# Optimization experiments

Hardware: AMD Instinct MI355X
Metric: run time of the kernel (lower is better)

## Reference

```python
import jax, jax.numpy as jnp
import numpy as np

B, T, D_IN, H, D_OUT = 256, 2048, 128, 128, 128


def setup_inputs() -> dict:
    key = jax.random.key(0)
    ks = jax.random.split(key, 7)
    s_in = 1.0 / np.sqrt(H)
    return {
        "x": jax.random.normal(ks[0], (B, T, D_IN), dtype=jnp.float32),
        "Wih": jax.random.normal(ks[1], (4 * H, D_IN), dtype=jnp.float32) * s_in,
        "Whh": jax.random.normal(ks[2], (4 * H, H), dtype=jnp.float32) * s_in,
        "bih": jax.random.normal(ks[3], (4 * H,), dtype=jnp.float32) * s_in,
        "bhh": jax.random.normal(ks[4], (4 * H,), dtype=jnp.float32) * s_in,
        "Wo": jax.random.normal(ks[5], (D_OUT, H), dtype=jnp.float32) * s_in,
        "bo": jax.random.normal(ks[6], (D_OUT,), dtype=jnp.float32) * s_in,
    }


def reference(x, Wih, Whh, bih, bhh, Wo, bo):
    # LSTM recurrence over time; module returns only the last step's
    # output projection (outputs[:, -1, :]).
    batch, seq_len, _ = x.shape
    h0 = jnp.zeros((batch, Whh.shape[1]), dtype=x.dtype)
    c0 = jnp.zeros_like(h0)
    # Precompute input-side gate projections for all timesteps in one GEMM.
    xg = jnp.einsum('btd,gd->btg', x, Wih) + bih + bhh  # [B, T, 4H]
    xg = jnp.swapaxes(xg, 0, 1)  # [T, B, 4H] for scan

    def step(carry, xg_t):
        h, c = carry
        gates = xg_t + h @ Whh.T  # [B, 4H]
        i, f, g, o = jnp.split(gates, 4, axis=-1)
        i = jax.nn.sigmoid(i)
        f = jax.nn.sigmoid(f)
        g = jnp.tanh(g)
        o = jax.nn.sigmoid(o)
        c = f * c + i * g
        h = o * jnp.tanh(c)
        return (h, c), None

    (h_last, _), _ = jax.lax.scan(step, (h0, c0), xg)
    return h_last @ Wo.T + bo  # [B, D_OUT]
```

## Files before the change

### kernel.cpp

```cpp
#include <hip/hip_runtime.h>
#include <hip/hip_fp16.h>

#define B_  256
#define T_  2048
#define D_  128
#define H_  128
#define CH  32
#define NCH (T_ / CH)

#define NLOG2E  (-1.4426950408889634f)
#define LOG2E2  ( 2.8853900817779268f)

typedef __attribute__((ext_vector_type(8))) _Float16 half8v;
typedef __attribute__((ext_vector_type(4))) float    floatx4;

static __device__ __forceinline__ unsigned pkh(float a, float b) {
  return __builtin_bit_cast(unsigned, __builtin_amdgcn_cvt_pkrtz(a, b));
}
static __device__ __forceinline__ float h2f_lo(unsigned u) {
  return __half2float(__ushort_as_half((unsigned short)(u & 0xffffu)));
}
static __device__ __forceinline__ float h2f_hi(unsigned u) {
  return __half2float(__ushort_as_half((unsigned short)(u >> 16)));
}
#define SEL4(v, n) (((n) & 2) ? (((n) & 1) ? (v)[3] : (v)[2]) \
                              : (((n) & 1) ? (v)[1] : (v)[0]))

__global__ __launch_bounds__(512, 2) void lstm_mfma(
    const float* __restrict__ x,   const float* __restrict__ Wih,
    const float* __restrict__ Whh, const float* __restrict__ bih,
    const float* __restrict__ bhh, const float* __restrict__ Wo,
    const float* __restrict__ bo,  float* __restrict__ out)
{
  __shared__ unsigned       xs[CH][68];
  __shared__ unsigned short xgf[CH][4 * H_];
  __shared__ __align__(16) unsigned hbuf[2][64];

  const int tid  = threadIdx.x;
  const int b    = blockIdx.x;
  const int lane = tid & 63;
  const int wv   = tid >> 6;
  const int quad = lane >> 4;
  const int m16  = lane & 15;

  uint4 wa[4][4];
  #pragma unroll
  for (int mt = 0; mt < 4; ++mt) {
    float s = (mt == 2) ? LOG2E2 : NLOG2E;
    const float4* p = (const float4*)(Whh + (size_t)(mt * 128 + wv * 16 + m16) * H_);
    #pragma unroll
    for (int kf = 0; kf < 4; ++kf) {
      float4 f0 = p[kf * 8 + quad * 2];
      float4 f1 = p[kf * 8 + quad * 2 + 1];
      uint4 u;
      u.x = pkh(f0.x * s, f0.y * s);  u.y = pkh(f0.z * s, f0.w * s);
      u.z = pkh(f1.x * s, f1.y * s);  u.w = pkh(f1.z * s, f1.w * s);
      wa[mt][kf] = u;
    }
  }

  const float sW = ((wv >> 1) == 2) ? LOG2E2 : NLOG2E;
  uint4 wb[4][4];
  float bv[4];
  #pragma unroll
  for (int nt = 0; nt < 4; ++nt) {
    int gcol = wv * 64 + nt * 16 + m16;
    const float4* p = (const float4*)(Wih + (size_t)gcol * D_);
    #pragma unroll
    for (int kf = 0; kf < 4; ++kf) {
      float4 f0 = p[kf * 8 + quad * 2];
      float4 f1 = p[kf * 8 + quad * 2 + 1];
      uint4 u;
      u.x = pkh(f0.x * sW, f0.y * sW);  u.y = pkh(f0.z * sW, f0.w * sW);
      u.z = pkh(f1.x * sW, f1.y * sW);  u.w = pkh(f1.z * sW, f1.w * sW);
      wb[nt][kf] = u;
    }
    bv[nt] = (bih[gcol] + bhh[gcol]) * sW;
  }

  if (tid < 128) hbuf[tid >> 6][tid & 63] = 0u;
  uint4 hfr[4] = {{0,0,0,0},{0,0,0,0},{0,0,0,0},{0,0,0,0}};
  float c = 0.0f;
  __syncthreads();

  const float* xb = x + (size_t)b * T_ * D_;

  for (int ch = 0; ch < NCH; ++ch) {
    const float4* xsrc = (const float4*)(xb + (size_t)ch * CH * D_);
    #pragma unroll
    for (int i = 0; i < 2; ++i) {
      int fi = i * 512 + tid;
      float4 v = xsrc[fi];
      int t  = fi >> 5;
      int kp = (fi & 31) * 2;
      xs[t][kp]     = pkh(v.x, v.y);
      xs[t][kp + 1] = pkh(v.z, v.w);
    }
    __syncthreads();

    #pragma unroll
    for (int mt = 0; mt < 2; ++mt) {
      half8v af[4];
      #pragma unroll
      for (int kf = 0; kf < 4; ++kf)
        af[kf] = __builtin_bit_cast(half8v,
                   *(const uint4*)&xs[mt * 16 + m16][kf * 16 + quad * 4]);
      #pragma unroll
      for (int nt = 0; nt < 4; ++nt) {
        floatx4 acc = {0.f, 0.f, 0.f, 0.f};
        #pragma unroll
        for (int kf = 0; kf < 4; ++kf)
          acc = __builtin_amdgcn_mfma_f32_16x16x32_f16(
              af[kf], __builtin_bit_cast(half8v, wb[nt][kf]), acc, 0, 0, 0);
        int gcol = wv * 64 + nt * 16 + m16;
        int jc   = gcol & 127, gt = gcol >> 7;
        #pragma unroll
        for (int r = 0; r < 4; ++r) {
          int trow = mt * 16 + quad * 4 + r;
          xgf[trow][jc * 4 + gt] =
              __half_as_ushort(__float2half(acc[r] + bv[nt]));
        }
      }
    }
    __syncthreads();

    for (int tt = 0; tt < CH; ++tt) {
      const int rp = (ch * CH + tt) & 1;
      unsigned long long xv = 0ull;
      if (m16 < 4) {
        xv = *(const unsigned long long*)&xgf[tt][(wv * 16 + quad * 4 + m16) * 4];
        #pragma unroll
        for (int kf = 0; kf < 4; ++kf)
          hfr[kf] = *(const uint4*)&hbuf[rp][kf * 16 + quad * 4];
      }
      floatx4 a0 = {0,0,0,0}, a1 = {0,0,0,0}, a2 = {0,0,0,0}, a3 = {0,0,0,0};
      #pragma unroll
      for (int kf = 0; kf < 4; ++kf) {
        half8v hb = __builtin_bit_cast(half8v, hfr[kf]);
        a0 = __builtin_amdgcn_mfma_f32_16x16x32_f16(
                 __builtin_bit_cast(half8v, wa[0][kf]), hb, a0, 0, 0, 0);
        a1 = __builtin_amdgcn_mfma_f32_16x16x32_f16(
                 __builtin_bit_cast(half8v, wa[1][kf]), hb, a1, 0, 0, 0);
        a2 = __builtin_amdgcn_mfma_f32_16x16x32_f16(
                 __builtin_bit_cast(half8v, wa[2][kf]), hb, a2, 0, 0, 0);
        a3 = __builtin_amdgcn_mfma_f32_16x16x32_f16(
                 __builtin_bit_cast(half8v, wa[3][kf]), hb, a3, 0, 0, 0);
      }
      if (m16 < 4) {
        const int n = m16;
        const int j = wv * 16 + quad * 4 + n;
        unsigned xlo = (unsigned)xv, xhi = (unsigned)(xv >> 32);
        float pi = SEL4(a0, n) + h2f_lo(xlo);
        float pf = SEL4(a1, n) + h2f_hi(xlo);
        float pg = SEL4(a2, n) + h2f_lo(xhi);
        float po = SEL4(a3, n) + h2f_hi(xhi);
        float gi = __builtin_amdgcn_rcpf(1.0f + __builtin_amdgcn_exp2f(pi));
        float gf = __builtin_amdgcn_rcpf(1.0f + __builtin_amdgcn_exp2f(pf));
        float go = __builtin_amdgcn_rcpf(1.0f + __builtin_amdgcn_exp2f(po));
        float gg = 1.0f - 2.0f * __builtin_amdgcn_rcpf(1.0f + __builtin_amdgcn_exp2f(pg));
        c = gf * c + gi * gg;
        float tc = 1.0f - 2.0f * __builtin_amdgcn_rcpf(
                       1.0f + __builtin_amdgcn_exp2f(c * LOG2E2));
        float h = go * tc;
        ((unsigned short*)hbuf[rp ^ 1])[j] = __half_as_ushort(__float2half(h));
      }
      __syncthreads();
    }
  }

  if (tid < H_) {
    float acc = bo[tid];
    const float4* wr = (const float4*)(Wo + (size_t)tid * H_);
    const uint2* hp = (const uint2*)hbuf[0];
    #pragma unroll
    for (int k4 = 0; k4 < 32; ++k4) {
      float4 w  = wr[k4];
      uint2  hu = hp[k4];
      acc += w.x * h2f_lo(hu.x) + w.y * h2f_hi(hu.x)
           + w.z * h2f_lo(hu.y) + w.w * h2f_hi(hu.y);
    }
    out[(size_t)b * H_ + tid] = acc;
  }
}

extern "C" void kernel_launch(void* const* d_in, const int* in_sizes, int n_in,
                              void* d_out, int out_size, void* d_ws, size_t ws_size,
                              hipStream_t stream) {
  (void)in_sizes; (void)n_in; (void)d_ws; (void)ws_size; (void)out_size;
  const float* x   = (const float*)d_in[0];
  const float* Wih = (const float*)d_in[1];
  const float* Whh = (const float*)d_in[2];
  const float* bih = (const float*)d_in[3];
  const float* bhh = (const float*)d_in[4];
  const float* Wo  = (const float*)d_in[5];
  const float* bo  = (const float*)d_in[6];
  lstm_mfma<<<B_, 512, 0, stream>>>(x, Wih, Whh, bih, bhh, Wo, bo, (float*)d_out);
}
```

Baseline: 1.315 ms.

## Split LSTM gate work across 16 waves with interleaved gate rows

Doubles the block to 1024 threads so each wave owns 8 hidden units instead of 16. Whh rows are interleaved by gate pairs, which cuts the per-step recurrent MFMAs per wave from 16 to 8 and halves the register-resident weights. The input projection is also split across more waves and reordered to share A fragments. This shortens the serial per-timestep critical path. In exchange, every per-step barrier now synchronises twice as many waves, and the launch bound of 4 blocks may squeeze registers.

```diff
diff --git a/kernel.cpp b/kernel.cpp
--- a/kernel.cpp
+++ b/kernel.cpp
@@ -23,10 +23,8 @@
 static __device__ __forceinline__ float h2f_hi(unsigned u) {
   return __half2float(__ushort_as_half((unsigned short)(u >> 16)));
 }
-#define SEL4(v, n) (((n) & 2) ? (((n) & 1) ? (v)[3] : (v)[2]) \
-                              : (((n) & 1) ? (v)[1] : (v)[0]))
 
-__global__ __launch_bounds__(512, 2) void lstm_mfma(
+__global__ __launch_bounds__(1024, 4) void lstm_mfma2(
     const float* __restrict__ x,   const float* __restrict__ Wih,
     const float* __restrict__ Whh, const float* __restrict__ bih,
     const float* __restrict__ bhh, const float* __restrict__ Wo,
@@ -40,36 +38,38 @@
   const int b    = blockIdx.x;
   const int lane = tid & 63;
   const int wv   = tid >> 6;
-  const int quad = lane >> 4;
+  const int quad = (lane >> 4);
   const int m16  = lane & 15;
 
-  uint4 wa[4][4];
+  uint4 wa[2][4];
   #pragma unroll
-  for (int mt = 0; mt < 4; ++mt) {
-    float s = (mt == 2) ? LOG2E2 : NLOG2E;
-    const float4* p = (const float4*)(Whh + (size_t)(mt * 128 + wv * 16 + m16) * H_);
+  for (int p = 0; p < 2; ++p) {
+    int gt  = p * 2 + (m16 & 1);
+    int row = gt * H_ + wv * 8 + (m16 >> 1);
+    float s = (gt == 2) ? LOG2E2 : NLOG2E;
+    const float4* pr = (const float4*)(Whh + (size_t)row * H_);
     #pragma unroll
     for (int kf = 0; kf < 4; ++kf) {
-      float4 f0 = p[kf * 8 + quad * 2];
-      float4 f1 = p[kf * 8 + quad * 2 + 1];
+      float4 f0 = pr[kf * 8 + quad * 2];
+      float4 f1 = pr[kf * 8 + quad * 2 + 1];
       uint4 u;
       u.x = pkh(f0.x * s, f0.y * s);  u.y = pkh(f0.z * s, f0.w * s);
       u.z = pkh(f1.x * s, f1.y * s);  u.w = pkh(f1.z * s, f1.w * s);
-      wa[mt][kf] = u;
+      wa[p][kf] = u;
     }
   }
 
-  const float sW = ((wv >> 1) == 2) ? LOG2E2 : NLOG2E;
-  uint4 wb[4][4];
-  float bv[4];
+  uint4 wb[2][4];
+  float bv[2];
   #pragma unroll
-  for (int nt = 0; nt < 4; ++nt) {
-    int gcol = wv * 64 + nt * 16 + m16;
-    const float4* p = (const float4*)(Wih + (size_t)gcol * D_);
+  for (int nt = 0; nt < 2; ++nt) {
+    int gcol = wv * 32 + nt * 16 + m16;
+    float sW = ((gcol >> 7) == 2) ? LOG2E2 : NLOG2E;
+    const float4* pr = (const float4*)(Wih + (size_t)gcol * D_);
     #pragma unroll
     for (int kf = 0; kf < 4; ++kf) {
-      float4 f0 = p[kf * 8 + quad * 2];
-      float4 f1 = p[kf * 8 + quad * 2 + 1];
+      float4 f0 = pr[kf * 8 + quad * 2];
+      float4 f1 = pr[kf * 8 + quad * 2 + 1];
       uint4 u;
       u.x = pkh(f0.x * sW, f0.y * sW);  u.y = pkh(f0.z * sW, f0.w * sW);
       u.z = pkh(f1.x * sW, f1.y * sW);  u.w = pkh(f1.z * sW, f1.w * sW);
@@ -86,54 +86,57 @@
   const float* xb = x + (size_t)b * T_ * D_;
 
   for (int ch = 0; ch < NCH; ++ch) {
-    const float4* xsrc = (const float4*)(xb + (size_t)ch * CH * D_);
-    #pragma unroll
-    for (int i = 0; i < 2; ++i) {
-      int fi = i * 512 + tid;
-      float4 v = xsrc[fi];
-      int t  = fi >> 5;
-      int kp = (fi & 31) * 2;
+    {
+      float4 v = ((const float4*)(xb + (size_t)ch * CH * D_))[tid];
+      int t  = tid >> 5;
+      int kp = (tid & 31) * 2;
       xs[t][kp]     = pkh(v.x, v.y);
       xs[t][kp + 1] = pkh(v.z, v.w);
     }
     __syncthreads();
 
-    #pragma unroll
-    for (int mt = 0; mt < 2; ++mt) {
-      half8v af[4];
+    {
+      floatx4 acc[2][2] = {{{0,0,0,0},{0,0,0,0}},{{0,0,0,0},{0,0,0,0}}};
       #pragma unroll
-      for (int kf = 0; kf < 4; ++kf)
-        af[kf] = __builtin_bit_cast(half8v,
-                   *(const uint4*)&xs[mt * 16 + m16][kf * 16 + quad * 4]);
+      for (int kf = 0; kf < 4; ++kf) {
+        half8v af[2];
+        #pragma unroll
+        for (int mt = 0; mt < 2; ++mt)
+          af[mt] = __builtin_bit_cast(half8v,
+                     *(const uint4*)&xs[mt * 16 + m16][kf * 16 + quad * 4]);
+        #pragma unroll
+        for (int mt = 0; mt < 2; ++mt)
+          #pragma unroll
+          for (int nt = 0; nt < 2; ++nt)
+            acc[mt][nt] = __builtin_amdgcn_mfma_f32_16x16x32_f16(
+                af[mt], __builtin_bit_cast(half8v, wb[nt][kf]), acc[mt][nt], 0, 0, 0);
+      }
       #pragma unroll
-      for (int nt = 0; nt < 4; ++nt) {
-        floatx4 acc = {0.f, 0.f, 0.f, 0.f};
+      for (int mt = 0; mt < 2; ++mt)
         #pragma unroll
-        for (int kf = 0; kf < 4; ++kf)
-          acc = __builtin_amdgcn_mfma_f32_16x16x32_f16(
-              af[kf], __builtin_bit_cast(half8v, wb[nt][kf]), acc, 0, 0, 0);
-        int gcol = wv * 64 + nt * 16 + m16;
-        int jc   = gcol & 127, gt = gcol >> 7;
-        #pragma unroll
-        for (int r = 0; r < 4; ++r) {
-          int trow = mt * 16 + quad * 4 + r;
-          xgf[trow][jc * 4 + gt] =
-              __half_as_ushort(__float2half(acc[r] + bv[nt]));
+        for (int nt = 0; nt < 2; ++nt) {
+          int gcol = wv * 32 + nt * 16 + m16;
+          int jc = gcol & 127, gt = gcol >> 7;
+          #pragma unroll
+          for (int r = 0; r < 4; ++r)
+            xgf[mt * 16 + quad * 4 + r][jc * 4 + gt] =
+                __half_as_ushort(__float2half(acc[mt][nt][r] + bv[nt]));
         }
-      }
     }
     __syncthreads();
 
+    #pragma unroll 2
     for (int tt = 0; tt < CH; ++tt) {
-      const int rp = (ch * CH + tt) & 1;
+      const int rp = tt & 1;
       unsigned long long xv = 0ull;
-      if (m16 < 4) {
-        xv = *(const unsigned long long*)&xgf[tt][(wv * 16 + quad * 4 + m16) * 4];
+      if (m16 < 2) {
+        int jl = wv * 8 + quad * 2 + m16;
+        xv = *(const unsigned long long*)&xgf[tt][jl * 4];
         #pragma unroll
         for (int kf = 0; kf < 4; ++kf)
           hfr[kf] = *(const uint4*)&hbuf[rp][kf * 16 + quad * 4];
       }
-      floatx4 a0 = {0,0,0,0}, a1 = {0,0,0,0}, a2 = {0,0,0,0}, a3 = {0,0,0,0};
+      floatx4 a0 = {0,0,0,0}, a1 = {0,0,0,0};
       #pragma unroll
       for (int kf = 0; kf < 4; ++kf) {
         half8v hb = __builtin_bit_cast(half8v, hfr[kf]);
@@ -141,19 +144,15 @@
                  __builtin_bit_cast(half8v, wa[0][kf]), hb, a0, 0, 0, 0);
         a1 = __builtin_amdgcn_mfma_f32_16x16x32_f16(
                  __builtin_bit_cast(half8v, wa[1][kf]), hb, a1, 0, 0, 0);
-        a2 = __builtin_amdgcn_mfma_f32_16x16x32_f16(
-                 __builtin_bit_cast(half8v, wa[2][kf]), hb, a2, 0, 0, 0);
-        a3 = __builtin_amdgcn_mfma_f32_16x16x32_f16(
-                 __builtin_bit_cast(half8v, wa[3][kf]), hb, a3, 0, 0, 0);
       }
-      if (m16 < 4) {
-        const int n = m16;
-        const int j = wv * 16 + quad * 4 + n;
+      if (m16 < 2) {
+        const int n  = m16;
+        const int jl = wv * 8 + quad * 2 + n;
         unsigned xlo = (unsigned)xv, xhi = (unsigned)(xv >> 32);
-        float pi = SEL4(a0, n) + h2f_lo(xlo);
-        float pf = SEL4(a1, n) + h2f_hi(xlo);
-        float pg = SEL4(a2, n) + h2f_lo(xhi);
-        float po = SEL4(a3, n) + h2f_hi(xhi);
+        float pi = (n ? a0[2] : a0[0]) + h2f_lo(xlo);
+        float pf = (n ? a0[3] : a0[1]) + h2f_hi(xlo);
+        float pg = (n ? a1[2] : a1[0]) + h2f_lo(xhi);
+        float po = (n ? a1[3] : a1[1]) + h2f_hi(xhi);
         float gi = __builtin_amdgcn_rcpf(1.0f + __builtin_amdgcn_exp2f(pi));
         float gf = __builtin_amdgcn_rcpf(1.0f + __builtin_amdgcn_exp2f(pf));
         float go = __builtin_amdgcn_rcpf(1.0f + __builtin_amdgcn_exp2f(po));
@@ -162,7 +161,7 @@
         float tc = 1.0f - 2.0f * __builtin_amdgcn_rcpf(
                        1.0f + __builtin_amdgcn_exp2f(c * LOG2E2));
         float h = go * tc;
-        ((unsigned short*)hbuf[rp ^ 1])[j] = __half_as_ushort(__float2half(h));
+        ((unsigned short*)hbuf[rp ^ 1])[jl] = __half_as_ushort(__float2half(h));
       }
       __syncthreads();
     }
@@ -194,5 +193,5 @@
   const float* bhh = (const float*)d_in[4];
   const float* Wo  = (const float*)d_in[5];
   const float* bo  = (const float*)d_in[6];
-  lstm_mfma<<<B_, 512, 0, stream>>>(x, Wih, Whh, bih, bhh, Wo, bo, (float*)d_out);
+  lstm_mfma2<<<B_, 1024, 0, stream>>>(x, Wih, Whh, bih, bhh, Wo, bo, (float*)d_out);
 }
```

After: 1.474 ms. +12.1%, slower.
